# Kernel tuning notes

Hardware: AMD Instinct MI355X
Metric: run time of the kernel (lower is better)

Reference implementation:

```python
import jax, jax.numpy as jnp
import numpy as np

BETA = 6.0
LOG_2PI = float(np.log(2.0 * np.pi))


def setup_inputs() -> dict:
    key = jax.random.key(0)
    k1, k2, k3, k4 = jax.random.split(key, 4)
    B, L = 2048, 64
    kl = jax.random.uniform(k1, (B, L), dtype=jnp.float32)
    z_mean = jax.random.normal(k2, (B, L), dtype=jnp.float32)
    z_logvar = jax.random.normal(k3, (B, L), dtype=jnp.float32)
    z_sampled = jax.random.normal(k4, (B, L), dtype=jnp.float32)
    return {"kl": kl, "z_mean": z_mean, "z_logvar": z_logvar, "z_sampled": z_sampled}


def gaussian_log_density(samples, mean, log_var):
    # samples: [B,1,L], mean/log_var: [1,B,L] -> [B,B,L]
    tmp = samples - mean
    return -0.5 * (tmp * tmp * jnp.exp(-log_var) + log_var + LOG_2PI)


def total_correlation(z, z_mean, z_logvar):
    # [B, B, L]: log q(z_i_l | x_j)
    log_qz_prob = gaussian_log_density(z[:, None, :], z_mean[None, :, :], z_logvar[None, :, :])
    # sum_l logsumexp_j -> [B]
    log_qz_product = jnp.sum(jax.scipy.special.logsumexp(log_qz_prob, axis=1), axis=1)
    # logsumexp_j sum_l -> [B]
    log_qz = jax.scipy.special.logsumexp(jnp.sum(log_qz_prob, axis=2), axis=1)
    return jnp.mean(log_qz - log_qz_product)


def reference(kl, z_mean, z_logvar, z_sampled):
    kl_loss = jnp.sum(kl)
    tc = (BETA - 1.0) * total_correlation(z_sampled, z_mean, z_logvar)
    return tc + kl_loss
```

## Files before the change

### kernel.cpp

```cpp
#include <hip/hip_runtime.h>
#include <math.h>


#define NB 2048
#define NL 64
#define NE (NB * NL)
#define BVAL 12.0f

__device__ __forceinline__ float wredsum(float v) {
#pragma unroll
  for (int o = 32; o; o >>= 1) v += __shfl_xor(v, o, 64);
  return v;
}
__device__ __forceinline__ float wredmax(float v) {
#pragma unroll
  for (int o = 32; o; o >>= 1) v = fmaxf(v, __shfl_xor(v, o, 64));
  return v;
}

__global__ __launch_bounds__(256) void k1_pre(const float* __restrict__ kl,
                                              const float* __restrict__ zm,
                                              const float* __restrict__ zlv,
                                              float2* __restrict__ PK2A,
                                              float* __restrict__ PK2B,
                                              float2* __restrict__ AM2T,
                                              float* __restrict__ QC2,
                                              float* __restrict__ KLP) {
  const float INVLN2 = 1.4426950408889634f;
  const float LOG2PI = 1.8378770664093453f;
  int tid = threadIdx.x;
  int e = blockIdx.x * 256 + tid;
  int j = e >> 6, l = e & 63;
  float lv = zlv[e], m = zm[e];
  float a2 = -0.5f * INVLN2 * __expf(-lv);
  float b2 = -0.5f * INVLN2 * (lv + LOG2PI);
  float c1 = -2.0f * a2 * m;
  float c0 = fmaf(a2 * m, m, b2);
  PK2A[e] = make_float2(a2, c1);
  PK2B[e] = c0 - BVAL;
  AM2T[l * NB + j] = make_float2(a2, c1);
  float q = wredsum(c0);
  if (l == 0) QC2[j] = q;
  float ks = wredsum(kl[e]);
  __shared__ float sk[4];
  if (l == 0) sk[tid >> 6] = ks;
  __syncthreads();
  if (tid == 0) KLP[blockIdx.x] = sk[0] + sk[1] + sk[2] + sk[3];
}

__global__ __launch_bounds__(256) void k23(const float* __restrict__ zs,
                                           const float2* __restrict__ AM2T,
                                           const float* __restrict__ QC2,
                                           const float2* __restrict__ PK2A,
                                           const float* __restrict__ PK2B,
                                           float* __restrict__ TPM,
                                           float* __restrict__ TPS,
                                           float* __restrict__ SP) {
  int jc = blockIdx.x;
  int y = blockIdx.y;
  int i0 = (y >> 1) * 8;
  int tid = threadIdx.x;
  int w = tid >> 6, l = tid & 63;

  if ((y & 1) == 0) {
    int j = jc * 256 + tid;
    __shared__ float zsh[64][8];
    if (tid < 128) {
      int k = tid >> 1, r0 = (tid & 1) * 4;
#pragma unroll
      for (int r = 0; r < 4; ++r) zsh[k][r0 + r] = zs[(i0 + r0 + r) * NL + k];
    }
    __syncthreads();
    float accv[8];
    float q = QC2[j];
#pragma unroll
    for (int r = 0; r < 8; ++r) accv[r] = q;
    for (int k = 0; k < 64; ++k) {
      float2 am = AM2T[k * NB + j];
      const float4* z4 = (const float4*)&zsh[k][0];
      float4 za = z4[0], zb = z4[1];
      float zk[8] = {za.x, za.y, za.z, za.w, zb.x, zb.y, zb.z, zb.w};
#pragma unroll
      for (int r = 0; r < 8; ++r) {
        accv[r] = fmaf(zk[r] * zk[r], am.x, accv[r]);
        accv[r] = fmaf(zk[r], am.y, accv[r]);
      }
    }
    __shared__ float lm[4][8], ls[4][8];
    float Mt[8];
#pragma unroll
    for (int r = 0; r < 8; ++r) {
      float mx = wredmax(accv[r]);
      if (l == 0) lm[w][r] = mx;
    }
    __syncthreads();
#pragma unroll
    for (int r = 0; r < 8; ++r)
      Mt[r] = fmaxf(fmaxf(lm[0][r], lm[1][r]), fmaxf(lm[2][r], lm[3][r]));
#pragma unroll
    for (int r = 0; r < 8; ++r) {
      float ss = wredsum(__builtin_amdgcn_exp2f(accv[r] - Mt[r]));
      if (l == 0) ls[w][r] = ss;
    }
    __syncthreads();
    if (tid == 0) {
#pragma unroll
      for (int r = 0; r < 8; ++r) {
        TPM[(i0 + r) * 8 + jc] = Mt[r];
        TPS[(i0 + r) * 8 + jc] = ls[0][r] + ls[1][r] + ls[2][r] + ls[3][r];
      }
    }
  } else {
    float zr[8];
#pragma unroll
    for (int r = 0; r < 8; ++r) zr[r] = zs[(i0 + r) * NL + l];
    float S[8];
#pragma unroll
    for (int r = 0; r < 8; ++r) S[r] = 0.0f;
    const float2* pa = PK2A + (size_t)(jc * 256 + w * 64) * NL + l;
    const float* pb = PK2B + (size_t)(jc * 256 + w * 64) * NL + l;
#pragma unroll 4
    for (int jj = 0; jj < 64; ++jj) {
      float2 c01 = pa[(size_t)jj * NL];
      float c2 = pb[(size_t)jj * NL];
#pragma unroll
      for (int r = 0; r < 8; ++r) {
        float lp2 = fmaf(fmaf(zr[r], c01.x, c01.y), zr[r], c2);
        S[r] += __builtin_amdgcn_exp2f(lp2);
      }
    }
    __shared__ float lss[4][8][64];
#pragma unroll
    for (int r = 0; r < 8; ++r) lss[w][r][l] = S[r];
    __syncthreads();
    for (int pp = tid; pp < 512; pp += 256) {
      int r = pp >> 6, ll = pp & 63;
      float Sc = lss[0][r][ll] + lss[1][r][ll] + lss[2][r][ll] + lss[3][r][ll];
      SP[((size_t)jc * NB + (i0 + r)) * NL + ll] = Sc;
    }
  }
}

__global__ __launch_bounds__(256) void k4_fin(const float* __restrict__ SP,
                                              const float* __restrict__ TPM,
                                              const float* __restrict__ TPS,
                                              float* __restrict__ PERI) {
  int tid = threadIdx.x;
  int w = tid >> 6, l = tid & 63;
  int i = blockIdx.x * 4 + w;
  float S = 0.0f;
#pragma unroll
  for (int s = 0; s < 8; ++s) S += SP[((size_t)s * NB + i) * NL + l];
  float val = __builtin_amdgcn_logf(S);
  float lqp2 = wredsum(val) + 64.0f * BVAL;
  float tm = (l < 8) ? TPM[i * 8 + l] : -1e30f;
  float ts = (l < 8) ? TPS[i * 8 + l] : 0.0f;
  float Mt = wredmax(tm);
  float St = wredsum(ts * __builtin_amdgcn_exp2f(tm - Mt));
  float lqz2 = Mt + __builtin_amdgcn_logf(St);
  if (l == 0) PERI[i] = lqz2 - lqp2;
}

__global__ __launch_bounds__(256) void k5_out(const float* __restrict__ KLP,
                                              const float* __restrict__ PERI,
                                              float* __restrict__ out) {
  int tid = threadIdx.x;
  float a = 0.0f, b = 0.0f;
  for (int x = tid; x < 512; x += 256) a += KLP[x];
  for (int x = tid; x < 2048; x += 256) b += PERI[x];
  float ra = wredsum(a), rb = wredsum(b);
  __shared__ float sa[4], sb[4];
  if ((tid & 63) == 0) {
    sa[tid >> 6] = ra;
    sb[tid >> 6] = rb;
  }
  __syncthreads();
  if (tid == 0) {
    const float LN2 = 0.6931471805599453f;
    float ka = sa[0] + sa[1] + sa[2] + sa[3];
    float kb = sb[0] + sb[1] + sb[2] + sb[3];
    out[0] = ka + 5.0f * LN2 * kb * (1.0f / (float)NB);
  }
}

extern "C" void kernel_launch(void* const* d_in, const int* in_sizes, int n_in,
                              void* d_out, int out_size, void* d_ws, size_t ws_size,
                              hipStream_t stream) {
  const float* kl = (const float*)d_in[0];
  const float* zm = (const float*)d_in[1];
  const float* zlv = (const float*)d_in[2];
  const float* zs = (const float*)d_in[3];
  float* ws = (float*)d_ws;

  float* PK2A = ws;
  float* PK2B = PK2A + 2 * NE;
  float* AM2T = PK2B + NE;
  float* QC2 = AM2T + 2 * NE;
  float* SP = QC2 + NB;
  float* TPM = SP + 8 * NE;
  float* TPS = TPM + NB * 8;
  float* KLP = TPS + NB * 8;
  float* PERI = KLP + 512;

  k1_pre<<<NE / 256, 256, 0, stream>>>(kl, zm, zlv, (float2*)PK2A, PK2B,
                                       (float2*)AM2T, QC2, KLP);
  k23<<<dim3(8, 2 * (NB / 8)), 256, 0, stream>>>(zs, (const float2*)AM2T, QC2,
                                                 (const float2*)PK2A, PK2B,
                                                 TPM, TPS, SP);
  k4_fin<<<NB / 4, 256, 0, stream>>>(SP, TPM, TPS, PERI);
  k5_out<<<1, 256, 0, stream>>>(KLP, PERI, (float*)d_out);
}
```

Measured before the change: 134.4 us.

## Merge the two k23 block roles into one block and pack coefficients as float4

Each k23 block now does both the joint-density logsumexp part and the per-dimension exp-sum part for the same 8 rows, instead of splitting them across alternating blocks. This halves the grid. The per-element coefficients are packed into a single float4 array so the inner loop issues one load instead of a float2 plus a float. Squared z values are also precomputed in shared memory. The merge lengthens each block and cuts parallelism, and the float4 padding adds 33% more coefficient bytes.

Measured after the change: 128.4 us. 4.5% less time.

```diff
diff --git a/kernel.cpp b/kernel.cpp
--- a/kernel.cpp
+++ b/kernel.cpp
@@ -21,8 +21,7 @@
 __global__ __launch_bounds__(256) void k1_pre(const float* __restrict__ kl,
                                               const float* __restrict__ zm,
                                               const float* __restrict__ zlv,
-                                              float2* __restrict__ PK2A,
-                                              float* __restrict__ PK2B,
+                                              float4* __restrict__ PK2,
                                               float2* __restrict__ AM2T,
                                               float* __restrict__ QC2,
                                               float* __restrict__ KLP) {
@@ -36,8 +35,7 @@
   float b2 = -0.5f * INVLN2 * (lv + LOG2PI);
   float c1 = -2.0f * a2 * m;
   float c0 = fmaf(a2 * m, m, b2);
-  PK2A[e] = make_float2(a2, c1);
-  PK2B[e] = c0 - BVAL;
+  PK2[e] = make_float4(a2, c1, c0 - BVAL, 0.0f);
   AM2T[l * NB + j] = make_float2(a2, c1);
   float q = wredsum(c0);
   if (l == 0) QC2[j] = q;
@@ -51,93 +49,96 @@
 __global__ __launch_bounds__(256) void k23(const float* __restrict__ zs,
                                            const float2* __restrict__ AM2T,
                                            const float* __restrict__ QC2,
-                                           const float2* __restrict__ PK2A,
-                                           const float* __restrict__ PK2B,
+                                           const float4* __restrict__ PK2,
                                            float* __restrict__ TPM,
                                            float* __restrict__ TPS,
                                            float* __restrict__ SP) {
   int jc = blockIdx.x;
-  int y = blockIdx.y;
-  int i0 = (y >> 1) * 8;
+  int i0 = blockIdx.y * 8;
   int tid = threadIdx.x;
   int w = tid >> 6, l = tid & 63;
-
-  if ((y & 1) == 0) {
-    int j = jc * 256 + tid;
-    __shared__ float zsh[64][8];
-    if (tid < 128) {
-      int k = tid >> 1, r0 = (tid & 1) * 4;
-#pragma unroll
-      for (int r = 0; r < 4; ++r) zsh[k][r0 + r] = zs[(i0 + r0 + r) * NL + k];
-    }
-    __syncthreads();
-    float accv[8];
-    float q = QC2[j];
-#pragma unroll
-    for (int r = 0; r < 8; ++r) accv[r] = q;
-    for (int k = 0; k < 64; ++k) {
-      float2 am = AM2T[k * NB + j];
-      const float4* z4 = (const float4*)&zsh[k][0];
-      float4 za = z4[0], zb = z4[1];
-      float zk[8] = {za.x, za.y, za.z, za.w, zb.x, zb.y, zb.z, zb.w};
-#pragma unroll
-      for (int r = 0; r < 8; ++r) {
-        accv[r] = fmaf(zk[r] * zk[r], am.x, accv[r]);
-        accv[r] = fmaf(zk[r], am.y, accv[r]);
-      }
-    }
-    __shared__ float lm[4][8], ls[4][8];
-    float Mt[8];
+  int j = jc * 256 + tid;
+
+  __shared__ float zsh[64][8];
+  __shared__ float zqh[64][8];
+  if (tid < 128) {
+    int k = tid >> 1, r0 = (tid & 1) * 4;
+#pragma unroll
+    for (int r = 0; r < 4; ++r) {
+      float z = zs[(i0 + r0 + r) * NL + k];
+      zsh[k][r0 + r] = z;
+      zqh[k][r0 + r] = z * z;
+    }
+  }
+  __syncthreads();
+
+  float accv[8];
+  float q = QC2[j];
+#pragma unroll
+  for (int r = 0; r < 8; ++r) accv[r] = q;
+  for (int k = 0; k < 64; ++k) {
+    float2 am = AM2T[k * NB + j];
+    const float4* z4 = (const float4*)&zsh[k][0];
+    const float4* q4 = (const float4*)&zqh[k][0];
+    float4 za = z4[0], zb = z4[1];
+    float4 qa = q4[0], qb = q4[1];
+    float zk[8] = {za.x, za.y, za.z, za.w, zb.x, zb.y, zb.z, zb.w};
+    float zz[8] = {qa.x, qa.y, qa.z, qa.w, qb.x, qb.y, qb.z, qb.w};
 #pragma unroll
     for (int r = 0; r < 8; ++r) {
-      float mx = wredmax(accv[r]);
-      if (l == 0) lm[w][r] = mx;
-    }
-    __syncthreads();
-#pragma unroll
-    for (int r = 0; r < 8; ++r)
-      Mt[r] = fmaxf(fmaxf(lm[0][r], lm[1][r]), fmaxf(lm[2][r], lm[3][r]));
+      accv[r] = fmaf(zz[r], am.x, accv[r]);
+      accv[r] = fmaf(zk[r], am.y, accv[r]);
+    }
+  }
+  __shared__ float lm[4][8], ls[4][8];
+  float Mt[8];
+#pragma unroll
+  for (int r = 0; r < 8; ++r) {
+    float mx = wredmax(accv[r]);
+    if (l == 0) lm[w][r] = mx;
+  }
+  __syncthreads();
+#pragma unroll
+  for (int r = 0; r < 8; ++r)
+    Mt[r] = fmaxf(fmaxf(lm[0][r], lm[1][r]), fmaxf(lm[2][r], lm[3][r]));
+#pragma unroll
+  for (int r = 0; r < 8; ++r) {
+    float ss = wredsum(__builtin_amdgcn_exp2f(accv[r] - Mt[r]));
+    if (l == 0) ls[w][r] = ss;
+  }
+  __syncthreads();
+  if (tid == 0) {
 #pragma unroll
     for (int r = 0; r < 8; ++r) {
-      float ss = wredsum(__builtin_amdgcn_exp2f(accv[r] - Mt[r]));
-      if (l == 0) ls[w][r] = ss;
-    }
-    __syncthreads();
-    if (tid == 0) {
-#pragma unroll
-      for (int r = 0; r < 8; ++r) {
-        TPM[(i0 + r) * 8 + jc] = Mt[r];
-        TPS[(i0 + r) * 8 + jc] = ls[0][r] + ls[1][r] + ls[2][r] + ls[3][r];
-      }
-    }
-  } else {
-    float zr[8];
-#pragma unroll
-    for (int r = 0; r < 8; ++r) zr[r] = zs[(i0 + r) * NL + l];
-    float S[8];
-#pragma unroll
-    for (int r = 0; r < 8; ++r) S[r] = 0.0f;
-    const float2* pa = PK2A + (size_t)(jc * 256 + w * 64) * NL + l;
-    const float* pb = PK2B + (size_t)(jc * 256 + w * 64) * NL + l;
+      TPM[(i0 + r) * 8 + jc] = Mt[r];
+      TPS[(i0 + r) * 8 + jc] = ls[0][r] + ls[1][r] + ls[2][r] + ls[3][r];
+    }
+  }
+
+  float zr[8];
+#pragma unroll
+  for (int r = 0; r < 8; ++r) zr[r] = zs[(i0 + r) * NL + l];
+  float S[8];
+#pragma unroll
+  for (int r = 0; r < 8; ++r) S[r] = 0.0f;
+  const float4* p = PK2 + (size_t)(jc * 256 + w * 64) * NL + l;
 #pragma unroll 4
-    for (int jj = 0; jj < 64; ++jj) {
-      float2 c01 = pa[(size_t)jj * NL];
-      float c2 = pb[(size_t)jj * NL];
-#pragma unroll
-      for (int r = 0; r < 8; ++r) {
-        float lp2 = fmaf(fmaf(zr[r], c01.x, c01.y), zr[r], c2);
-        S[r] += __builtin_amdgcn_exp2f(lp2);
-      }
-    }
-    __shared__ float lss[4][8][64];
-#pragma unroll
-    for (int r = 0; r < 8; ++r) lss[w][r][l] = S[r];
-    __syncthreads();
-    for (int pp = tid; pp < 512; pp += 256) {
-      int r = pp >> 6, ll = pp & 63;
-      float Sc = lss[0][r][ll] + lss[1][r][ll] + lss[2][r][ll] + lss[3][r][ll];
-      SP[((size_t)jc * NB + (i0 + r)) * NL + ll] = Sc;
-    }
+  for (int jj = 0; jj < 64; ++jj) {
+    float4 c = p[(size_t)jj * NL];
+#pragma unroll
+    for (int r = 0; r < 8; ++r) {
+      float lp2 = fmaf(fmaf(zr[r], c.x, c.y), zr[r], c.z);
+      S[r] += __builtin_amdgcn_exp2f(lp2);
+    }
+  }
+  __shared__ float lss[4][8][64];
+#pragma unroll
+  for (int r = 0; r < 8; ++r) lss[w][r][l] = S[r];
+  __syncthreads();
+  for (int pp = tid; pp < 512; pp += 256) {
+    int r = pp >> 6, ll = pp & 63;
+    float Sc = lss[0][r][ll] + lss[1][r][ll] + lss[2][r][ll] + lss[3][r][ll];
+    SP[((size_t)jc * NB + (i0 + r)) * NL + ll] = Sc;
   }
 }
 
@@ -192,9 +193,8 @@
   const float* zs = (const float*)d_in[3];
   float* ws = (float*)d_ws;
 
-  float* PK2A = ws;
-  float* PK2B = PK2A + 2 * NE;
-  float* AM2T = PK2B + NE;
+  float* PK2 = ws;
+  float* AM2T = PK2 + 4 * NE;
   float* QC2 = AM2T + 2 * NE;
   float* SP = QC2 + NB;
   float* TPM = SP + 8 * NE;
@@ -202,11 +202,10 @@
   float* KLP = TPS + NB * 8;
   float* PERI = KLP + 512;
 
-  k1_pre<<<NE / 256, 256, 0, stream>>>(kl, zm, zlv, (float2*)PK2A, PK2B,
+  k1_pre<<<NE / 256, 256, 0, stream>>>(kl, zm, zlv, (float4*)PK2,
                                        (float2*)AM2T, QC2, KLP);
-  k23<<<dim3(8, 2 * (NB / 8)), 256, 0, stream>>>(zs, (const float2*)AM2T, QC2,
-                                                 (const float2*)PK2A, PK2B,
-                                                 TPM, TPS, SP);
+  k23<<<dim3(8, NB / 8), 256, 0, stream>>>(zs, (const float2*)AM2T, QC2,
+                                           (const float4*)PK2, TPM, TPS, SP);
   k4_fin<<<NB / 4, 256, 0, stream>>>(SP, TPM, TPS, PERI);
   k5_out<<<1, 256, 0, stream>>>(KLP, PERI, (float*)d_out);
 }
```
